# Optimization experiments

Measured on AMD Instinct MI355X. Metric: run time of the kernel, lower is better.

Reference implementation:

```python
import jax, jax.numpy as jnp
import numpy as np

EPS = 1e-4

def softmax_kernel(data, proj, is_query):
    # FAVOR+ positive softmax random features; data: [b,h,l,d], proj: [d,m]
    d = data.shape[-1]
    m = proj.shape[-1]
    data_normalizer = d ** -0.25  # normalize_data=True
    ratio = m ** -0.5
    data_dash = jnp.einsum('bhld,dm->bhlm', data, proj) * data_normalizer
    diag = 0.5 * jnp.sum(data * data, axis=-1, keepdims=True) * (data_normalizer ** 2)
    if is_query:
        stab = jnp.max(data_dash, axis=-1, keepdims=True)   # per-token max
    else:
        stab = jnp.max(data_dash, axis=(-2, -1), keepdims=True)  # per (b,h) max
    out = ratio * (jnp.exp(data_dash - diag - stab) + EPS)
    return out, stab

def low_mem_attn(qp, kp, v, causal, chunk):
    # qp,kp: [b,h,l,m] positive features; v: [b,h,l,d]
    b, h, l, m = qp.shape
    d = v.shape[-1]
    if not causal:
        kv = jnp.einsum('bhlm,bhld->bhmd', kp, v)
        den = jnp.einsum('bhlm,bhm->bhl', qp, jnp.sum(kp, axis=2))
        return jnp.einsum('bhlm,bhmd->bhld', qp, kv) / den[..., None]
    nc = l // chunk
    qc = qp.reshape(b, h, nc, chunk, m)
    kc = kp.reshape(b, h, nc, chunk, m)
    vc = v.reshape(b, h, nc, chunk, d)
    # intra-chunk causal part
    mask = jnp.tril(jnp.ones((chunk, chunk), dtype=qp.dtype))
    scores = jnp.einsum('bhcim,bhcjm->bhcij', qc, kc) * mask
    intra = jnp.einsum('bhcij,bhcjd->bhcid', scores, vc)
    intra_den = jnp.sum(scores, axis=-1)  # [b,h,nc,chunk]
    # inter-chunk via exclusive cumulative sums of KV state
    kv = jnp.einsum('bhcjm,bhcjd->bhcmd', kc, vc)          # per-chunk KV
    kv_prev = jnp.cumsum(kv, axis=2) - kv                   # exclusive cumsum
    ks = jnp.sum(kc, axis=3)                                # [b,h,nc,m]
    ks_prev = jnp.cumsum(ks, axis=2) - ks
    inter = jnp.einsum('bhcim,bhcmd->bhcid', qc, kv_prev)
    inter_den = jnp.einsum('bhcim,bhcm->bhci', qc, ks_prev)
    out = (intra + inter) / (intra_den + inter_den)[..., None]
    return out.reshape(b, h, l, d)


def setup_inputs() -> dict:
    key = jax.random.key(0)
    k1, k2, k3, k4 = jax.random.split(key, 4)
    B, H, L, D, M = 2, 16, 4096, 64, 64
    return {
        'q': jax.random.normal(k1, (B, H, L, D), dtype=jnp.float32),
        'k': jax.random.normal(k2, (B, H, L, D), dtype=jnp.float32),
        'v': jax.random.normal(k3, (B, H, L, D), dtype=jnp.float32),
        'projection_matrix': jax.random.normal(k4, (D, M), dtype=jnp.float32),
        'chunk_size': 128,
    }


def reference(q, k, v, projection_matrix, chunk_size):
    qp, _ = softmax_kernel(q, projection_matrix, is_query=True)
    kp, _key_maxima = softmax_kernel(k, projection_matrix, is_query=False)
    o = low_mem_attn(qp, kp, v, causal=True, chunk=chunk_size)
    return o
```

## Files before the change

### kernel.cpp

```cpp
#include <hip/hip_runtime.h>
#include <hip/hip_bf16.h>

#define TPB 256
#define ATPB 512

constexpr int   Bc = 2, Hc = 16, Lc = 4096, Dc = 64, Mc = 64, CHc = 128;
constexpr int   NCc = Lc / CHc;
constexpr int   BHc = Bc * Hc;
constexpr float DNF    = 0.35355339059327373f;
constexpr float RATIOF = 0.125f;
constexpr float EPSF   = 1e-4f;

constexpr long QP_OFF  = 0;
constexpr long KP_OFF  = 4194304;
constexpr long KPB_OFF = 12582912;
constexpr long VTB_OFF = 16777216;
constexpr long KV_OFF  = 20971520;
constexpr long KVB_OFF = 25165824;
constexpr long KS_OFF  = 27262976;
constexpr long HM_OFF  = 27328512;

typedef __attribute__((ext_vector_type(8))) short bf16x8;
typedef __attribute__((ext_vector_type(4))) float f32x4;

__device__ __forceinline__ unsigned fordmap(float f) {
  unsigned u = __float_as_uint(f);
  return (u & 0x80000000u) ? ~u : (u | 0x80000000u);
}
__device__ __forceinline__ float fordunmap(unsigned u) {
  return __uint_as_float((u & 0x80000000u) ? (u & 0x7fffffffu) : ~u);
}
__device__ __forceinline__ unsigned pk2(float a, float b) {
  union { __hip_bfloat16 h; unsigned short u; } ca, cb;
  ca.h = __float2bfloat16(a); cb.h = __float2bfloat16(b);
  return ((unsigned)cb.u << 16) | (unsigned)ca.u;
}
__device__ __forceinline__ short f2bf(float a) {
  union { __hip_bfloat16 h; short s; } c; c.h = __float2bfloat16(a); return c.s;
}
__device__ __forceinline__ float bf2f(short s) {
  return __uint_as_float(((unsigned)(unsigned short)s) << 16);
}

__global__ void k_init(unsigned* hmax) {
  int t = threadIdx.x;
  if (t < BHc) hmax[t] = 0u;
}

template <bool IS_Q>
__global__ __launch_bounds__(TPB) void k_feat(const float* __restrict__ x,
                                              const float* __restrict__ P,
                                              float* __restrict__ outf,
                                              short* __restrict__ outb,
                                              unsigned* __restrict__ hmax) {
  __shared__ short xb[128 * 72];
  __shared__ short Pt[64 * 72];
  __shared__ float od[128 * 68];
  __shared__ float diag_s[128];
  __shared__ unsigned bmax_s;
  const int t = threadIdx.x;
  const long rowbase = (long)blockIdx.x * 128;
  for (int i = t; i < 4096; i += TPB) {
    const int r = i >> 5, d2 = (i & 31) * 2;
    float2 xv = *(const float2*)&x[rowbase * 64 + r * 64 + d2];
    *(unsigned*)&xb[r * 72 + d2] = pk2(xv.x, xv.y);
  }
  for (int i = t; i < 4096; i += TPB) {
    const int d = i >> 6, m = i & 63;
    Pt[m * 72 + d] = f2bf(P[i]);
  }
  if (t == 0) bmax_s = 0u;
  {
    const int row = t >> 1, half = t & 1;
    float s = 0.f;
#pragma unroll
    for (int d = 0; d < 32; d += 4) {
      float4 vv = *(const float4*)&x[(rowbase + row) * 64 + half * 32 + d];
      s += vv.x * vv.x + vv.y * vv.y + vv.z * vv.z + vv.w * vv.w;
    }
    s += __shfl_xor(s, 1);
    if (half == 0) diag_s[row] = 0.0625f * s;
  }
  __syncthreads();

  const int w = t >> 6, lane = t & 63;
  const int lrow = lane & 15, quad = lane >> 4;
  float tmax = -1e30f;
#pragma unroll
  for (int rt2 = 0; rt2 < 2; ++rt2) {
    const int rt = w * 2 + rt2;
    const bf16x8 a0 = *(const bf16x8*)&xb[(rt * 16 + lrow) * 72 + quad * 8];
    const bf16x8 a1 = *(const bf16x8*)&xb[(rt * 16 + lrow) * 72 + 32 + quad * 8];
    f32x4 c[4];
#pragma unroll
    for (int ct = 0; ct < 4; ++ct) {
      const bf16x8 b0 = *(const bf16x8*)&Pt[(ct * 16 + lrow) * 72 + quad * 8];
      const bf16x8 b1 = *(const bf16x8*)&Pt[(ct * 16 + lrow) * 72 + 32 + quad * 8];
      f32x4 cc = {0.f, 0.f, 0.f, 0.f};
      cc = __builtin_amdgcn_mfma_f32_16x16x32_bf16(a0, b0, cc, 0, 0, 0);
      cc = __builtin_amdgcn_mfma_f32_16x16x32_bf16(a1, b1, cc, 0, 0, 0);
#pragma unroll
      for (int r = 0; r < 4; ++r) cc[r] *= DNF;
      c[ct] = cc;
    }
    if constexpr (IS_Q) {
      short* ob = (short*)od;
#pragma unroll
      for (int r = 0; r < 4; ++r) {
        float mx = fmaxf(fmaxf(c[0][r], c[1][r]), fmaxf(c[2][r], c[3][r]));
#pragma unroll
        for (int off = 1; off < 16; off <<= 1) mx = fmaxf(mx, __shfl_xor(mx, off));
        const int row = rt * 16 + quad * 4 + r;
        const float dg = diag_s[row];
#pragma unroll
        for (int ct = 0; ct < 4; ++ct)
          ob[row * 64 + ct * 16 + lrow] =
              f2bf(RATIOF * (expf(c[ct][r] - dg - mx) + EPSF));
      }
    } else {
#pragma unroll
      for (int r = 0; r < 4; ++r) {
        const int row = rt * 16 + quad * 4 + r;
        const float dg = diag_s[row];
#pragma unroll
        for (int ct = 0; ct < 4; ++ct) {
          tmax = fmaxf(tmax, c[ct][r]);
          od[row * 68 + ct * 16 + lrow] = c[ct][r] - dg;
        }
      }
    }
  }
  if constexpr (!IS_Q) {
#pragma unroll
    for (int off = 1; off < 64; off <<= 1) tmax = fmaxf(tmax, __shfl_xor(tmax, off));
    if (lane == 0) atomicMax(&bmax_s, fordmap(tmax));
  }
  __syncthreads();
  if constexpr (IS_Q) {
    const short* ob = (const short*)od;
    for (int i = t; i < 1024; i += TPB)
      *(uint4*)&outb[rowbase * 64 + i * 8] = *(const uint4*)&ob[i * 8];
  } else {
    for (int i = t; i < 2048; i += TPB) {
      const int row = i >> 4, c4 = (i & 15) * 4;
      *(float4*)&outf[rowbase * 64 + row * 64 + c4] = *(const float4*)&od[row * 68 + c4];
    }
    if (t == 0) atomicMax(&hmax[rowbase >> 12], bmax_s);
  }
}

__global__ __launch_bounds__(TPB) void k_ckv(const float* __restrict__ kp,
                                             const float* __restrict__ v,
                                             float* __restrict__ kvT,
                                             float* __restrict__ ks,
                                             short* __restrict__ kpb,
                                             short* __restrict__ vtb,
                                             const unsigned* __restrict__ hmax) {
  __shared__ short Kt[64 * 136];
  __shared__ short Vt[64 * 136];
  __shared__ float ks_s[64];
  const int t = threadIdx.x;
  const int bhc = blockIdx.x;
  const long base = (long)bhc * 8192;
  const float stab = fordunmap(hmax[bhc >> 5]);
  if (t < 64) ks_s[t] = 0.f;
  __syncthreads();
  {
    const int m2 = (t & 31) * 2;
    float s0 = 0.f, s1 = 0.f;
    for (int i = t; i < 4096; i += TPB) {
      const int j = i >> 5;
      float2 kk = *(const float2*)&kp[base + j * 64 + m2];
      const float e0 = RATIOF * (expf(kk.x - stab) + EPSF);
      const float e1 = RATIOF * (expf(kk.y - stab) + EPSF);
      *(unsigned*)&kpb[base + j * 64 + m2] = pk2(e0, e1);
      Kt[m2 * 136 + j] = f2bf(e0);
      Kt[(m2 + 1) * 136 + j] = f2bf(e1);
      s0 += e0; s1 += e1;
    }
    atomicAdd(&ks_s[m2], s0);
    atomicAdd(&ks_s[m2 + 1], s1);
  }
  {
    const int d2 = (t & 31) * 2;
    for (int i = t; i < 4096; i += TPB) {
      const int j = i >> 5;
      float2 vv = *(const float2*)&v[base + j * 64 + d2];
      Vt[d2 * 136 + j] = f2bf(vv.x);
      Vt[(d2 + 1) * 136 + j] = f2bf(vv.y);
    }
  }
  __syncthreads();
  for (int i = t; i < 1024; i += TPB) {
    const int d = i >> 4, c8 = (i & 15) * 8;
    *(uint4*)&vtb[base + d * 128 + c8] = *(const uint4*)&Vt[d * 136 + c8];
  }
  if (t < 64) ks[bhc * 64 + t] = ks_s[t];
  const int w = t >> 6, lane = t & 63;
  const int lrow = lane & 15, quad = lane >> 4;
  f32x4 acc[4];
#pragma unroll
  for (int mt = 0; mt < 4; ++mt) acc[mt] = (f32x4){0.f, 0.f, 0.f, 0.f};
#pragma unroll
  for (int ksq = 0; ksq < 4; ++ksq) {
    const bf16x8 a = *(const bf16x8*)&Vt[(w * 16 + lrow) * 136 + ksq * 32 + quad * 8];
#pragma unroll
    for (int mt = 0; mt < 4; ++mt) {
      const bf16x8 b = *(const bf16x8*)&Kt[(mt * 16 + lrow) * 136 + ksq * 32 + quad * 8];
      acc[mt] = __builtin_amdgcn_mfma_f32_16x16x32_bf16(a, b, acc[mt], 0, 0, 0);
    }
  }
  const long kvb = (long)bhc * 4096;
#pragma unroll
  for (int mt = 0; mt < 4; ++mt)
#pragma unroll
    for (int r = 0; r < 4; ++r)
      kvT[kvb + (long)(w * 16 + quad * 4 + r) * 64 + mt * 16 + lrow] = acc[mt][r];
}

__global__ void k_scan(const float* __restrict__ kv, short* __restrict__ kvb,
                       float* __restrict__ ks) {
  if (blockIdx.x < 512) {
    const int tid = blockIdx.x * TPB + threadIdx.x;
    const int bh = tid >> 12, rem = tid & 4095;
    float run = 0.f;
    for (int c = 0; c < NCc; ++c) {
      const long idx = ((long)(bh * NCc + c)) * 4096 + rem;
      kvb[idx] = f2bf(run);
      run += kv[idx];
    }
  } else {
    for (int tid = threadIdx.x; tid < BHc * 64; tid += TPB) {
      const int bh = tid >> 6, m = tid & 63;
      float run = 0.f;
      for (int c = 0; c < NCc; ++c) {
        const int idx = (bh * NCc + c) * 64 + m;
        const float val = ks[idx];
        ks[idx] = run;
        run += val;
      }
    }
  }
}

__global__ __launch_bounds__(ATPB, 4) void k_attn(const short* __restrict__ qpb,
                                                  const short* __restrict__ kpb,
                                                  const short* __restrict__ vtb,
                                                  const short* __restrict__ kvb,
                                                  const float* __restrict__ ksp,
                                                  float* __restrict__ outp) {
  __shared__ short Ks[128 * 72];
  __shared__ short Vt[64 * 136];
  __shared__ short KVt[64 * 72];
  __shared__ short Ps[128 * 136];
  __shared__ float kss[64];
  __shared__ float dens[128];
  const int t = threadIdx.x;
  const int bhc = blockIdx.x;
  const long cbase = (long)bhc * 8192;

  for (int i = t; i < 1024; i += ATPB) {
    const int r = i >> 3, c8 = (i & 7) * 8;
    *(uint4*)&Ks[r * 72 + c8] = *(const uint4*)&kpb[cbase + r * 64 + c8];
  }
  for (int i = t; i < 1024; i += ATPB) {
    const int d = i >> 4, c8 = (i & 15) * 8;
    *(uint4*)&Vt[d * 136 + c8] = *(const uint4*)&vtb[cbase + d * 128 + c8];
  }
  {
    const int d = t >> 3, c8 = (t & 7) * 8;
    *(uint4*)&KVt[d * 72 + c8] = *(const uint4*)&kvb[(long)bhc * 4096 + d * 64 + c8];
  }
  if (t < 64) kss[t] = ksp[bhc * 64 + t];
  for (int i = t; i < 1024; i += ATPB) {
    const int tp = i >> 8, rr = (i >> 4) & 15, cc = i & 15;
    Ps[(tp * 32 + rr) * 136 + tp * 32 + 16 + cc] = 0;
  }
  const int w = t >> 6, lane = t & 63;
  const int lrow = lane & 15, quad = lane >> 4;
  const int ri = w;
  const long qrb = cbase + (long)(ri * 16 + lrow) * 64;
  const bf16x8 a0 = *(const bf16x8*)&qpb[qrb + quad * 8];
  const bf16x8 a1 = *(const bf16x8*)&qpb[qrb + 32 + quad * 8];
  __syncthreads();

  float qks = 0.f;
#pragma unroll
  for (int j = 0; j < 8; ++j) {
    qks += bf2f(a0[j]) * kss[quad * 8 + j];
    qks += bf2f(a1[j]) * kss[32 + quad * 8 + j];
  }
  qks += __shfl_xor(qks, 16);
  qks += __shfl_xor(qks, 32);
  if (quad == 0) dens[ri * 16 + lrow] = qks;

  float rs0 = 0.f, rs1 = 0.f, rs2 = 0.f, rs3 = 0.f;
  for (int cj = 0; cj <= ri; ++cj) {
    const bf16x8 b0 = *(const bf16x8*)&Ks[(cj * 16 + lrow) * 72 + quad * 8];
    const bf16x8 b1 = *(const bf16x8*)&Ks[(cj * 16 + lrow) * 72 + 32 + quad * 8];
    f32x4 c = {0.f, 0.f, 0.f, 0.f};
    c = __builtin_amdgcn_mfma_f32_16x16x32_bf16(a0, b0, c, 0, 0, 0);
    c = __builtin_amdgcn_mfma_f32_16x16x32_bf16(a1, b1, c, 0, 0, 0);
    if (cj == ri) {
#pragma unroll
      for (int r = 0; r < 4; ++r)
        if (lrow > quad * 4 + r) c[r] = 0.f;
    }
    const int colb = cj * 16 + lrow;
    Ps[(ri * 16 + quad * 4 + 0) * 136 + colb] = f2bf(c[0]); rs0 += c[0];
    Ps[(ri * 16 + quad * 4 + 1) * 136 + colb] = f2bf(c[1]); rs1 += c[1];
    Ps[(ri * 16 + quad * 4 + 2) * 136 + colb] = f2bf(c[2]); rs2 += c[2];
    Ps[(ri * 16 + quad * 4 + 3) * 136 + colb] = f2bf(c[3]); rs3 += c[3];
  }
#pragma unroll
  for (int off = 1; off < 16; off <<= 1) {
    rs0 += __shfl_xor(rs0, off);
    rs1 += __shfl_xor(rs1, off);
    rs2 += __shfl_xor(rs2, off);
    rs3 += __shfl_xor(rs3, off);
  }
  if (lrow == 0) {
    dens[ri * 16 + quad * 4 + 0] += rs0;
    dens[ri * 16 + quad * 4 + 1] += rs1;
    dens[ri * 16 + quad * 4 + 2] += rs2;
    dens[ri * 16 + quad * 4 + 3] += rs3;
  }

  f32x4 acc0 = {0.f,0.f,0.f,0.f}, acc1 = {0.f,0.f,0.f,0.f};
  f32x4 acc2 = {0.f,0.f,0.f,0.f}, acc3 = {0.f,0.f,0.f,0.f};
  const int nj = (ri + 2) >> 1;
  for (int jc = 0; jc < nj; ++jc) {
    const bf16x8 a  = *(const bf16x8*)&Ps[(ri * 16 + lrow) * 136 + jc * 32 + quad * 8];
    const bf16x8 b0 = *(const bf16x8*)&Vt[(lrow) * 136 + jc * 32 + quad * 8];
    const bf16x8 b1 = *(const bf16x8*)&Vt[(16 + lrow) * 136 + jc * 32 + quad * 8];
    const bf16x8 b2 = *(const bf16x8*)&Vt[(32 + lrow) * 136 + jc * 32 + quad * 8];
    const bf16x8 b3 = *(const bf16x8*)&Vt[(48 + lrow) * 136 + jc * 32 + quad * 8];
    acc0 = __builtin_amdgcn_mfma_f32_16x16x32_bf16(a, b0, acc0, 0, 0, 0);
    acc1 = __builtin_amdgcn_mfma_f32_16x16x32_bf16(a, b1, acc1, 0, 0, 0);
    acc2 = __builtin_amdgcn_mfma_f32_16x16x32_bf16(a, b2, acc2, 0, 0, 0);
    acc3 = __builtin_amdgcn_mfma_f32_16x16x32_bf16(a, b3, acc3, 0, 0, 0);
  }
  {
    const bf16x8 b0 = *(const bf16x8*)&KVt[(lrow) * 72 + quad * 8];
    const bf16x8 b1 = *(const bf16x8*)&KVt[(16 + lrow) * 72 + quad * 8];
    const bf16x8 b2 = *(const bf16x8*)&KVt[(32 + lrow) * 72 + quad * 8];
    const bf16x8 b3 = *(const bf16x8*)&KVt[(48 + lrow) * 72 + quad * 8];
    acc0 = __builtin_amdgcn_mfma_f32_16x16x32_bf16(a0, b0, acc0, 0, 0, 0);
    acc1 = __builtin_amdgcn_mfma_f32_16x16x32_bf16(a0, b1, acc1, 0, 0, 0);
    acc2 = __builtin_amdgcn_mfma_f32_16x16x32_bf16(a0, b2, acc2, 0, 0, 0);
    acc3 = __builtin_amdgcn_mfma_f32_16x16x32_bf16(a0, b3, acc3, 0, 0, 0);
    const bf16x8 c0 = *(const bf16x8*)&KVt[(lrow) * 72 + 32 + quad * 8];
    const bf16x8 c1 = *(const bf16x8*)&KVt[(16 + lrow) * 72 + 32 + quad * 8];
    const bf16x8 c2 = *(const bf16x8*)&KVt[(32 + lrow) * 72 + 32 + quad * 8];
    const bf16x8 c3 = *(const bf16x8*)&KVt[(48 + lrow) * 72 + 32 + quad * 8];
    acc0 = __builtin_amdgcn_mfma_f32_16x16x32_bf16(a1, c0, acc0, 0, 0, 0);
    acc1 = __builtin_amdgcn_mfma_f32_16x16x32_bf16(a1, c1, acc1, 0, 0, 0);
    acc2 = __builtin_amdgcn_mfma_f32_16x16x32_bf16(a1, c2, acc2, 0, 0, 0);
    acc3 = __builtin_amdgcn_mfma_f32_16x16x32_bf16(a1, c3, acc3, 0, 0, 0);
  }
#pragma unroll
  for (int r = 0; r < 4; ++r) {
    const int row = ri * 16 + quad * 4 + r;
    const float inv = 1.f / dens[row];
    const long ob = cbase + (long)row * 64 + lrow;
    outp[ob]      = acc0[r] * inv;
    outp[ob + 16] = acc1[r] * inv;
    outp[ob + 32] = acc2[r] * inv;
    outp[ob + 48] = acc3[r] * inv;
  }
}

extern "C" void kernel_launch(void* const* d_in, const int* in_sizes, int n_in,
                              void* d_out, int out_size, void* d_ws, size_t ws_size,
                              hipStream_t stream) {
  const float* q = (const float*)d_in[0];
  const float* k = (const float*)d_in[1];
  const float* v = (const float*)d_in[2];
  const float* P = (const float*)d_in[3];
  float* ws = (float*)d_ws;
  short*    qpb  = (short*)(ws + QP_OFF);
  float*    kp   = ws + KP_OFF;
  short*    kpb  = (short*)(ws + KPB_OFF);
  short*    vtb  = (short*)(ws + VTB_OFF);
  float*    kvT  = ws + KV_OFF;
  short*    kvb  = (short*)(ws + KVB_OFF);
  float*    ks   = ws + KS_OFF;
  unsigned* hmax = (unsigned*)(ws + HM_OFF);
  float* out = (float*)d_out;

  k_init<<<1, 64, 0, stream>>>(hmax);
  k_feat<true><<<dim3(1024), dim3(TPB), 0, stream>>>(q, P, nullptr, qpb, nullptr);
  k_feat<false><<<dim3(1024), dim3(TPB), 0, stream>>>(k, P, kp, nullptr, hmax);
  k_ckv<<<dim3(1024), dim3(TPB), 0, stream>>>(kp, v, kvT, ks, kpb, vtb, hmax);
  k_scan<<<dim3(513), dim3(TPB), 0, stream>>>(kvT, kvb, ks);
  k_attn<<<dim3(1024), dim3(ATPB), 0, stream>>>(qpb, kpb, vtb, kvb, ks, out);
}
```

Measured before the change: 213.4 us.

## Recompute key projection instead of storing fp32 key features to workspace

The key feature pass is split into a max-only kernel (k_stab) that computes the projection and reduces the per-head maximum without writing anything, and a fused k_kv kernel that recomputes the projection from raw k and then does exp, feature-sum, transposition and KV product. This removes the 32 MB fp32 intermediate write and its re-read, at the cost of running the k@P MFMA twice and reading k twice. The kpb output is now packed from the transposed LDS tile.

Result: no change. 210.0 us (-1.6%).

```diff
diff --git a/kernel.cpp b/kernel.cpp
--- a/kernel.cpp
+++ b/kernel.cpp
@@ -12,13 +12,12 @@
 constexpr float EPSF   = 1e-4f;
 
 constexpr long QP_OFF  = 0;
-constexpr long KP_OFF  = 4194304;
-constexpr long KPB_OFF = 12582912;
-constexpr long VTB_OFF = 16777216;
-constexpr long KV_OFF  = 20971520;
-constexpr long KVB_OFF = 25165824;
-constexpr long KS_OFF  = 27262976;
-constexpr long HM_OFF  = 27328512;
+constexpr long KPB_OFF = 4194304;
+constexpr long VTB_OFF = 8388608;
+constexpr long KV_OFF  = 12582912;
+constexpr long KVB_OFF = 16777216;
+constexpr long KS_OFF  = 18874368;
+constexpr long HM_OFF  = 18939904;
 
 typedef __attribute__((ext_vector_type(8))) short bf16x8;
 typedef __attribute__((ext_vector_type(4))) float f32x4;
@@ -47,17 +46,13 @@
   if (t < BHc) hmax[t] = 0u;
 }
 
-template <bool IS_Q>
-__global__ __launch_bounds__(TPB) void k_feat(const float* __restrict__ x,
-                                              const float* __restrict__ P,
-                                              float* __restrict__ outf,
-                                              short* __restrict__ outb,
-                                              unsigned* __restrict__ hmax) {
+__global__ __launch_bounds__(TPB) void k_featq(const float* __restrict__ x,
+                                               const float* __restrict__ P,
+                                               short* __restrict__ outb) {
   __shared__ short xb[128 * 72];
   __shared__ short Pt[64 * 72];
-  __shared__ float od[128 * 68];
+  __shared__ short ob[128 * 64];
   __shared__ float diag_s[128];
-  __shared__ unsigned bmax_s;
   const int t = threadIdx.x;
   const long rowbase = (long)blockIdx.x * 128;
   for (int i = t; i < 4096; i += TPB) {
@@ -69,7 +64,6 @@
     const int d = i >> 6, m = i & 63;
     Pt[m * 72 + d] = f2bf(P[i]);
   }
-  if (t == 0) bmax_s = 0u;
   {
     const int row = t >> 1, half = t & 1;
     float s = 0.f;
@@ -85,7 +79,6 @@
 
   const int w = t >> 6, lane = t & 63;
   const int lrow = lane & 15, quad = lane >> 4;
-  float tmax = -1e30f;
 #pragma unroll
   for (int rt2 = 0; rt2 < 2; ++rt2) {
     const int rt = w * 2 + rt2;
@@ -103,83 +96,96 @@
       for (int r = 0; r < 4; ++r) cc[r] *= DNF;
       c[ct] = cc;
     }
-    if constexpr (IS_Q) {
-      short* ob = (short*)od;
-#pragma unroll
-      for (int r = 0; r < 4; ++r) {
-        float mx = fmaxf(fmaxf(c[0][r], c[1][r]), fmaxf(c[2][r], c[3][r]));
-#pragma unroll
-        for (int off = 1; off < 16; off <<= 1) mx = fmaxf(mx, __shfl_xor(mx, off));
-        const int row = rt * 16 + quad * 4 + r;
-        const float dg = diag_s[row];
-#pragma unroll
-        for (int ct = 0; ct < 4; ++ct)
-          ob[row * 64 + ct * 16 + lrow] =
-              f2bf(RATIOF * (expf(c[ct][r] - dg - mx) + EPSF));
-      }
-    } else {
-#pragma unroll
-      for (int r = 0; r < 4; ++r) {
-        const int row = rt * 16 + quad * 4 + r;
-        const float dg = diag_s[row];
-#pragma unroll
-        for (int ct = 0; ct < 4; ++ct) {
-          tmax = fmaxf(tmax, c[ct][r]);
-          od[row * 68 + ct * 16 + lrow] = c[ct][r] - dg;
-        }
-      }
-    }
-  }
-  if constexpr (!IS_Q) {
-#pragma unroll
-    for (int off = 1; off < 64; off <<= 1) tmax = fmaxf(tmax, __shfl_xor(tmax, off));
-    if (lane == 0) atomicMax(&bmax_s, fordmap(tmax));
-  }
-  __syncthreads();
-  if constexpr (IS_Q) {
-    const short* ob = (const short*)od;
-    for (int i = t; i < 1024; i += TPB)
-      *(uint4*)&outb[rowbase * 64 + i * 8] = *(const uint4*)&ob[i * 8];
-  } else {
-    for (int i = t; i < 2048; i += TPB) {
-      const int row = i >> 4, c4 = (i & 15) * 4;
-      *(float4*)&outf[rowbase * 64 + row * 64 + c4] = *(const float4*)&od[row * 68 + c4];
-    }
-    if (t == 0) atomicMax(&hmax[rowbase >> 12], bmax_s);
-  }
-}
-
-__global__ __launch_bounds__(TPB) void k_ckv(const float* __restrict__ kp,
-                                             const float* __restrict__ v,
-                                             float* __restrict__ kvT,
-                                             float* __restrict__ ks,
-                                             short* __restrict__ kpb,
-                                             short* __restrict__ vtb,
-                                             const unsigned* __restrict__ hmax) {
+#pragma unroll
+    for (int r = 0; r < 4; ++r) {
+      float mx = fmaxf(fmaxf(c[0][r], c[1][r]), fmaxf(c[2][r], c[3][r]));
+#pragma unroll
+      for (int off = 1; off < 16; off <<= 1) mx = fmaxf(mx, __shfl_xor(mx, off));
+      const int row = rt * 16 + quad * 4 + r;
+      const float dg = diag_s[row];
+#pragma unroll
+      for (int ct = 0; ct < 4; ++ct)
+        ob[row * 64 + ct * 16 + lrow] =
+            f2bf(RATIOF * (expf(c[ct][r] - dg - mx) + EPSF));
+    }
+  }
+  __syncthreads();
+  for (int i = t; i < 1024; i += TPB)
+    *(uint4*)&outb[rowbase * 64 + i * 8] = *(const uint4*)&ob[i * 8];
+}
+
+__global__ __launch_bounds__(TPB) void k_stab(const float* __restrict__ kin,
+                                              const float* __restrict__ P,
+                                              unsigned* __restrict__ hmax) {
+  __shared__ short kb[128 * 72];
+  __shared__ short Pt[64 * 72];
+  __shared__ unsigned bmax_s;
+  const int t = threadIdx.x;
+  const long base = (long)blockIdx.x * 8192;
+  if (t == 0) bmax_s = 0u;
+  for (int i = t; i < 4096; i += TPB) {
+    const int r = i >> 5, d2 = (i & 31) * 2;
+    float2 kk = *(const float2*)&kin[base + r * 64 + d2];
+    *(unsigned*)&kb[r * 72 + d2] = pk2(kk.x, kk.y);
+  }
+  for (int i = t; i < 4096; i += TPB) {
+    const int d = i >> 6, m = i & 63;
+    Pt[m * 72 + d] = f2bf(P[i]);
+  }
+  __syncthreads();
+  const int w = t >> 6, lane = t & 63;
+  const int lrow = lane & 15, quad = lane >> 4;
+  float tmax = -1e30f;
+#pragma unroll
+  for (int rt2 = 0; rt2 < 2; ++rt2) {
+    const int rt = w * 2 + rt2;
+    const bf16x8 a0 = *(const bf16x8*)&kb[(rt * 16 + lrow) * 72 + quad * 8];
+    const bf16x8 a1 = *(const bf16x8*)&kb[(rt * 16 + lrow) * 72 + 32 + quad * 8];
+#pragma unroll
+    for (int ct = 0; ct < 4; ++ct) {
+      const bf16x8 b0 = *(const bf16x8*)&Pt[(ct * 16 + lrow) * 72 + quad * 8];
+      const bf16x8 b1 = *(const bf16x8*)&Pt[(ct * 16 + lrow) * 72 + 32 + quad * 8];
+      f32x4 cc = {0.f, 0.f, 0.f, 0.f};
+      cc = __builtin_amdgcn_mfma_f32_16x16x32_bf16(a0, b0, cc, 0, 0, 0);
+      cc = __builtin_amdgcn_mfma_f32_16x16x32_bf16(a1, b1, cc, 0, 0, 0);
+#pragma unroll
+      for (int r = 0; r < 4; ++r) tmax = fmaxf(tmax, cc[r] * DNF);
+    }
+  }
+#pragma unroll
+  for (int off = 1; off < 64; off <<= 1) tmax = fmaxf(tmax, __shfl_xor(tmax, off));
+  if (lane == 0) atomicMax(&bmax_s, fordmap(tmax));
+  __syncthreads();
+  if (t == 0) atomicMax(&hmax[blockIdx.x >> 5], bmax_s);
+}
+
+__global__ __launch_bounds__(TPB) void k_kv(const float* __restrict__ kin,
+                                            const float* __restrict__ v,
+                                            const float* __restrict__ P,
+                                            float* __restrict__ kvT,
+                                            float* __restrict__ ks,
+                                            short* __restrict__ kpb,
+                                            short* __restrict__ vtb,
+                                            const unsigned* __restrict__ hmax) {
+  __shared__ short kb[128 * 72];
+  __shared__ short Pt[64 * 72];
   __shared__ short Kt[64 * 136];
   __shared__ short Vt[64 * 136];
+  __shared__ float diag_s[128];
   __shared__ float ks_s[64];
   const int t = threadIdx.x;
   const int bhc = blockIdx.x;
   const long base = (long)bhc * 8192;
   const float stab = fordunmap(hmax[bhc >> 5]);
   if (t < 64) ks_s[t] = 0.f;
-  __syncthreads();
-  {
-    const int m2 = (t & 31) * 2;
-    float s0 = 0.f, s1 = 0.f;
-    for (int i = t; i < 4096; i += TPB) {
-      const int j = i >> 5;
-      float2 kk = *(const float2*)&kp[base + j * 64 + m2];
-      const float e0 = RATIOF * (expf(kk.x - stab) + EPSF);
-      const float e1 = RATIOF * (expf(kk.y - stab) + EPSF);
-      *(unsigned*)&kpb[base + j * 64 + m2] = pk2(e0, e1);
-      Kt[m2 * 136 + j] = f2bf(e0);
-      Kt[(m2 + 1) * 136 + j] = f2bf(e1);
-      s0 += e0; s1 += e1;
-    }
-    atomicAdd(&ks_s[m2], s0);
-    atomicAdd(&ks_s[m2 + 1], s1);
+  for (int i = t; i < 4096; i += TPB) {
+    const int r = i >> 5, d2 = (i & 31) * 2;
+    float2 kk = *(const float2*)&kin[base + r * 64 + d2];
+    *(unsigned*)&kb[r * 72 + d2] = pk2(kk.x, kk.y);
+  }
+  for (int i = t; i < 4096; i += TPB) {
+    const int d = i >> 6, m = i & 63;
+    Pt[m * 72 + d] = f2bf(P[i]);
   }
   {
     const int d2 = (t & 31) * 2;
@@ -190,14 +196,70 @@
       Vt[(d2 + 1) * 136 + j] = f2bf(vv.y);
     }
   }
+  {
+    const int row = t >> 1, half = t & 1;
+    float s = 0.f;
+#pragma unroll
+    for (int d = 0; d < 32; d += 4) {
+      float4 vv = *(const float4*)&kin[base + row * 64 + half * 32 + d];
+      s += vv.x * vv.x + vv.y * vv.y + vv.z * vv.z + vv.w * vv.w;
+    }
+    s += __shfl_xor(s, 1);
+    if (half == 0) diag_s[row] = 0.0625f * s;
+  }
   __syncthreads();
   for (int i = t; i < 1024; i += TPB) {
     const int d = i >> 4, c8 = (i & 15) * 8;
     *(uint4*)&vtb[base + d * 128 + c8] = *(const uint4*)&Vt[d * 136 + c8];
   }
-  if (t < 64) ks[bhc * 64 + t] = ks_s[t];
   const int w = t >> 6, lane = t & 63;
   const int lrow = lane & 15, quad = lane >> 4;
+  float ksp_[4] = {0.f, 0.f, 0.f, 0.f};
+#pragma unroll
+  for (int rt2 = 0; rt2 < 2; ++rt2) {
+    const int rt = w * 2 + rt2;
+    const bf16x8 a0 = *(const bf16x8*)&kb[(rt * 16 + lrow) * 72 + quad * 8];
+    const bf16x8 a1 = *(const bf16x8*)&kb[(rt * 16 + lrow) * 72 + 32 + quad * 8];
+#pragma unroll
+    for (int ct = 0; ct < 4; ++ct) {
+      const bf16x8 b0 = *(const bf16x8*)&Pt[(ct * 16 + lrow) * 72 + quad * 8];
+      const bf16x8 b1 = *(const bf16x8*)&Pt[(ct * 16 + lrow) * 72 + 32 + quad * 8];
+      f32x4 cc = {0.f, 0.f, 0.f, 0.f};
+      cc = __builtin_amdgcn_mfma_f32_16x16x32_bf16(a0, b0, cc, 0, 0, 0);
+      cc = __builtin_amdgcn_mfma_f32_16x16x32_bf16(a1, b1, cc, 0, 0, 0);
+      const int m = ct * 16 + lrow;
+#pragma unroll
+      for (int r = 0; r < 4; ++r) {
+        const int row = rt * 16 + quad * 4 + r;
+        const float e = RATIOF * (expf(cc[r] * DNF - diag_s[row] - stab) + EPSF);
+        Kt[m * 136 + row] = f2bf(e);
+        ksp_[ct] += e;
+      }
+    }
+  }
+#pragma unroll
+  for (int ct = 0; ct < 4; ++ct) {
+    ksp_[ct] += __shfl_xor(ksp_[ct], 16);
+    ksp_[ct] += __shfl_xor(ksp_[ct], 32);
+  }
+  if (quad == 0) {
+#pragma unroll
+    for (int ct = 0; ct < 4; ++ct) atomicAdd(&ks_s[ct * 16 + lrow], ksp_[ct]);
+  }
+  __syncthreads();
+  if (t < 64) ks[bhc * 64 + t] = ks_s[t];
+  for (int i = t; i < 1024; i += TPB) {
+    const int j = i >> 3, m8 = (i & 7) * 8;
+    unsigned u[4];
+#pragma unroll
+    for (int p = 0; p < 4; ++p) {
+      const unsigned lo = (unsigned short)Kt[(m8 + 2 * p) * 136 + j];
+      const unsigned hi = (unsigned short)Kt[(m8 + 2 * p + 1) * 136 + j];
+      u[p] = lo | (hi << 16);
+    }
+    uint4 w4; w4.x = u[0]; w4.y = u[1]; w4.z = u[2]; w4.w = u[3];
+    *(uint4*)&kpb[base + j * 64 + m8] = w4;
+  }
   f32x4 acc[4];
 #pragma unroll
   for (int mt = 0; mt < 4; ++mt) acc[mt] = (f32x4){0.f, 0.f, 0.f, 0.f};
@@ -210,12 +272,12 @@
       acc[mt] = __builtin_amdgcn_mfma_f32_16x16x32_bf16(a, b, acc[mt], 0, 0, 0);
     }
   }
-  const long kvb = (long)bhc * 4096;
+  const long kvo = (long)bhc * 4096;
 #pragma unroll
   for (int mt = 0; mt < 4; ++mt)
 #pragma unroll
     for (int r = 0; r < 4; ++r)
-      kvT[kvb + (long)(w * 16 + quad * 4 + r) * 64 + mt * 16 + lrow] = acc[mt][r];
+      kvT[kvo + (long)(w * 16 + quad * 4 + r) * 64 + mt * 16 + lrow] = acc[mt][r];
 }
 
 __global__ void k_scan(const float* __restrict__ kv, short* __restrict__ kvb,
@@ -379,7 +441,6 @@
   const float* P = (const float*)d_in[3];
   float* ws = (float*)d_ws;
   short*    qpb  = (short*)(ws + QP_OFF);
-  float*    kp   = ws + KP_OFF;
   short*    kpb  = (short*)(ws + KPB_OFF);
   short*    vtb  = (short*)(ws + VTB_OFF);
   float*    kvT  = ws + KV_OFF;
@@ -389,9 +450,9 @@
   float* out = (float*)d_out;
 
   k_init<<<1, 64, 0, stream>>>(hmax);
-  k_feat<true><<<dim3(1024), dim3(TPB), 0, stream>>>(q, P, nullptr, qpb, nullptr);
-  k_feat<false><<<dim3(1024), dim3(TPB), 0, stream>>>(k, P, kp, nullptr, hmax);
-  k_ckv<<<dim3(1024), dim3(TPB), 0, stream>>>(kp, v, kvT, ks, kpb, vtb, hmax);
+  k_featq<<<dim3(1024), dim3(TPB), 0, stream>>>(q, P, qpb);
+  k_stab<<<dim3(1024), dim3(TPB), 0, stream>>>(k, P, hmax);
+  k_kv<<<dim3(1024), dim3(TPB), 0, stream>>>(k, v, P, kvT, ks, kpb, vtb, hmax);
   k_scan<<<dim3(513), dim3(TPB), 0, stream>>>(kvT, kvb, ks);
   k_attn<<<dim3(1024), dim3(ATPB), 0, stream>>>(qpb, kpb, vtb, kvb, ks, out);
 }
```
